# Kernel optimization log

Measured on AMD Instinct MI355X. Metric: run time of the kernel, lower is better.

The kernel has to match this reference:

```python
import jax, jax.numpy as jnp
import numpy as np

B, N, F_IN, F_OUT = 8, 2048, 256, 128
ALPHA = 0.2  # LeakyReLU negative slope (smooth=False)
MASK_VAL = -9e15


def setup_inputs() -> dict:
    key = jax.random.key(0)
    k1, k2, k3, k4 = jax.random.split(key, 4)
    h = jax.random.normal(k1, (B, N, F_IN), dtype=jnp.float32)
    adj = jax.random.randint(k2, (B, N, N), 0, 2, dtype=jnp.int32)
    # xavier_uniform with gain=1.414 ~ U(-b, b), b = gain*sqrt(6/(fan_in+fan_out))
    bW = 1.414 * np.sqrt(6.0 / (F_IN + F_OUT))
    W = jax.random.uniform(k3, (F_IN, F_OUT), minval=-bW, maxval=bW, dtype=jnp.float32)
    ba = 1.414 * np.sqrt(6.0 / (2 * F_OUT + 1))
    a = jax.random.uniform(k4, (2 * F_OUT, 1), minval=-ba, maxval=ba, dtype=jnp.float32)
    return {"h": h, "adj": adj, "W": W, "a": a}


def reference(h, adj, W, a):
    Wh = jnp.einsum('bni,io->bno', h, W)              # [B,N,F_OUT]
    fo = Wh.shape[-1]
    a1 = a[:fo, 0]                                    # attends to source i
    a2 = a[fo:, 0]                                    # attends to target j
    # e[b,i,j] = leaky_relu(Wh[b,i]@a1 + Wh[b,j]@a2) — equivalent to the
    # concat([Wh_i, Wh_j]) @ a construction without the O(N^2 * 2F) tensor.
    s1 = Wh @ a1                                      # [B,N]
    s2 = Wh @ a2                                      # [B,N]
    e = jax.nn.leaky_relu(s1[:, :, None] + s2[:, None, :], negative_slope=ALPHA)
    att = jnp.where(adj > 0, e, MASK_VAL)
    att = jax.nn.softmax(att, axis=-1)                # [B,N,N]
    # dropout is identity in eval mode (training=False)
    h_prime = jnp.einsum('bij,bjo->bio', att, Wh)     # [B,N,F_OUT]
    return jax.nn.elu(h_prime)                        # concat=True path
```

## Files before the change

kernel.cpp:

```cpp
#include <hip/hip_runtime.h>
#include <math.h>

#define Bn 8
#define Nn 2048
#define FIn 256
#define FOn 128

typedef __attribute__((ext_vector_type(8))) short short8;
typedef __attribute__((ext_vector_type(4))) float f32x4;
typedef __attribute__((ext_vector_type(4))) unsigned short ushort4v;

__device__ __forceinline__ unsigned short f2bf(float x){
    union { float f; unsigned u; } v; v.f = x;
    unsigned r = v.u + 0x7fffu + ((v.u >> 16) & 1u);
    return (unsigned short)(r >> 16);
}

__global__ void k0_wt(const float* __restrict__ W, unsigned short* __restrict__ WT){
    int o = blockIdx.x, k = threadIdx.x;
    WT[o*FIn + k] = f2bf(W[k*FOn + o]);
}

__global__ __launch_bounds__(256) void k1_gemm(const float* __restrict__ h,
        const unsigned short* __restrict__ WT, const float* __restrict__ a,
        unsigned short* __restrict__ WhT, float* __restrict__ s1, float* __restrict__ s2){
    __shared__ __align__(16) unsigned short tr[128][48];
    __shared__ float ps1[2][32], ps2[2][32];
    int t = threadIdx.x, lane = t & 63, w = t >> 6;
    int rg = w >> 1, ch = w & 1;
    int l16 = lane & 15, khalf = (lane >> 4) * 8;
    long g0 = (long)blockIdx.x * 32;
    int b = (int)(g0 >> 11);
    int i0 = (int)(g0 & 2047);
    long row = g0 + rg*16 + l16;
    f32x4 acc[4];
    #pragma unroll
    for (int nf=0;nf<4;nf++) acc[nf] = (f32x4){0.f,0.f,0.f,0.f};
    #pragma unroll
    for (int ks=0; ks<8; ks++){
        int kb = ks*32 + khalf;
        const float4* hp = (const float4*)(h + row*FIn + kb);
        float4 h0 = hp[0], h1 = hp[1];
        short8 af;
        af[0]=(short)f2bf(h0.x); af[1]=(short)f2bf(h0.y); af[2]=(short)f2bf(h0.z); af[3]=(short)f2bf(h0.w);
        af[4]=(short)f2bf(h1.x); af[5]=(short)f2bf(h1.y); af[6]=(short)f2bf(h1.z); af[7]=(short)f2bf(h1.w);
        #pragma unroll
        for (int nf=0;nf<4;nf++){
            short8 bfv = *(const short8*)(WT + (ch*64 + nf*16 + l16)*FIn + kb);
            acc[nf] = __builtin_amdgcn_mfma_f32_16x16x32_bf16(af, bfv, acc[nf], 0, 0, 0);
        }
    }
    {
        float a1v[4], a2v[4];
        #pragma unroll
        for (int nf=0;nf<4;nf++){
            a1v[nf] = a[ch*64 + nf*16 + l16];
            a2v[nf] = a[FOn + ch*64 + nf*16 + l16];
        }
        #pragma unroll
        for (int r=0;r<4;r++){
            float u1 = 0.f, u2 = 0.f;
            #pragma unroll
            for (int nf=0;nf<4;nf++){ u1 = fmaf(acc[nf][r], a1v[nf], u1); u2 = fmaf(acc[nf][r], a2v[nf], u2); }
            u1 += __shfl_xor(u1, 1); u1 += __shfl_xor(u1, 2); u1 += __shfl_xor(u1, 4); u1 += __shfl_xor(u1, 8);
            u2 += __shfl_xor(u2, 1); u2 += __shfl_xor(u2, 2); u2 += __shfl_xor(u2, 4); u2 += __shfl_xor(u2, 8);
            if (l16 == 0){
                int rloc = rg*16 + ((lane>>4)<<2) + r;
                ps1[ch][rloc] = u1; ps2[ch][rloc] = u2;
            }
        }
    }
    int rbase = rg*16 + ((lane>>4)<<2);
    #pragma unroll
    for (int nf=0;nf<4;nf++)
        #pragma unroll
        for (int r=0;r<4;r++)
            tr[ch*64 + nf*16 + l16][rbase + r] = f2bf(acc[nf][r]);
    __syncthreads();
    if (t < 32){
        s1[g0 + t] = ps1[0][t] + ps1[1][t];
        s2[g0 + t] = ps2[0][t] + ps2[1][t];
    }
    int o = t >> 1, seg = t & 1;
    short8 v0 = *(const short8*)&tr[o][seg*16];
    short8 v1 = *(const short8*)&tr[o][seg*16 + 8];
    unsigned short* dst = WhT + ((long)(b*FOn + o))*Nn + i0 + seg*16;
    *(short8*)(dst)     = v0;
    *(short8*)(dst + 8) = v1;
}

__global__ __launch_bounds__(512) void k3_flash(const int* __restrict__ adj,
        const unsigned short* __restrict__ WhT, const float* __restrict__ s1g,
        const float* __restrict__ s2g, float* __restrict__ out){
    __shared__ __align__(16) unsigned short pt[2][32][72];
    __shared__ float m_s[32], l_s[32], rs_s[2][32];
    int t = threadIdx.x, lane = t & 63, w = t >> 6;
    int bid = blockIdx.x;
    int b = bid & 7;
    int i0 = (bid >> 3) * 32;
    int q = t >> 4;
    int c = t & 15;
    int rg = w >> 2, cq = w & 3;
    int l16 = lane & 15, khalf = (lane >> 4) * 8;
    if (t < 32){ m_s[t] = -INFINITY; l_s[t] = 0.f; }
    f32x4 acc[2];
    acc[0] = (f32x4){0.f,0.f,0.f,0.f};
    acc[1] = (f32x4){0.f,0.f,0.f,0.f};
    float s1r = s1g[b*Nn + i0 + q];
    const int* ajbase = adj + ((long)(b*Nn + i0 + q))*Nn + c*4;
    const float* s2base = s2g + b*Nn + c*4;
    const unsigned short* Bbase = WhT + ((long)(b*FOn + cq*32 + l16))*Nn + khalf;
    int4 ajA = *(const int4*)(ajbase + 0*64);
    int4 ajB = *(const int4*)(ajbase + 1*64);
    __syncthreads();

#define SCORE_TILE(AJREG, PAR, J0)                                              \
    {                                                                           \
        int4 av = AJREG;                                                        \
        int jn2 = (J0) + 128;  jn2 = jn2 < Nn ? jn2 : Nn - 64;                  \
        AJREG = *(const int4*)(ajbase + jn2);                                   \
        float4 s2c = *(const float4*)(s2base + (J0));                           \
        float sc0 = s1r + s2c.x; sc0 = sc0 > 0.f ? sc0 : 0.2f*sc0; sc0 = av.x > 0 ? sc0 : -9e15f; \
        float sc1 = s1r + s2c.y; sc1 = sc1 > 0.f ? sc1 : 0.2f*sc1; sc1 = av.y > 0 ? sc1 : -9e15f; \
        float sc2 = s1r + s2c.z; sc2 = sc2 > 0.f ? sc2 : 0.2f*sc2; sc2 = av.z > 0 ? sc2 : -9e15f; \
        float sc3 = s1r + s2c.w; sc3 = sc3 > 0.f ? sc3 : 0.2f*sc3; sc3 = av.w > 0 ? sc3 : -9e15f; \
        float tm = fmaxf(fmaxf(sc0, sc1), fmaxf(sc2, sc3));                     \
        tm = fmaxf(tm, __shfl_xor(tm, 1));                                      \
        tm = fmaxf(tm, __shfl_xor(tm, 2));                                      \
        tm = fmaxf(tm, __shfl_xor(tm, 4));                                      \
        tm = fmaxf(tm, __shfl_xor(tm, 8));                                      \
        float mo = m_s[q];                                                      \
        float mn = fmaxf(mo, tm);                                               \
        float rsc = __expf(mo - mn);                                            \
        float p0 = __expf(sc0 - mn), p1 = __expf(sc1 - mn);                     \
        float p2 = __expf(sc2 - mn), p3 = __expf(sc3 - mn);                     \
        float ps = (p0+p1)+(p2+p3);                                             \
        ps += __shfl_xor(ps, 1); ps += __shfl_xor(ps, 2);                       \
        ps += __shfl_xor(ps, 4); ps += __shfl_xor(ps, 8);                       \
        if (c == 0){ m_s[q] = mn; l_s[q] = l_s[q]*rsc + ps; rs_s[PAR][q] = rsc; } \
        ushort4v pv;                                                            \
        pv[0] = f2bf(p0); pv[1] = f2bf(p1); pv[2] = f2bf(p2); pv[3] = f2bf(p3); \
        *(ushort4v*)&pt[PAR][q][c*4] = pv;                                      \
    }

#define MFMA_TILE(PAR, J0)                                                      \
    {                                                                           \
        __syncthreads();                                                        \
        float rv0 = rs_s[PAR][rg*16 + ((lane>>4)<<2) + 0];                      \
        float rv1 = rs_s[PAR][rg*16 + ((lane>>4)<<2) + 1];                      \
        float rv2 = rs_s[PAR][rg*16 + ((lane>>4)<<2) + 2];                      \
        float rv3 = rs_s[PAR][rg*16 + ((lane>>4)<<2) + 3];                      \
        acc[0][0]*=rv0; acc[0][1]*=rv1; acc[0][2]*=rv2; acc[0][3]*=rv3;         \
        acc[1][0]*=rv0; acc[1][1]*=rv1; acc[1][2]*=rv2; acc[1][3]*=rv3;         \
        const unsigned short* Bp = Bbase + (J0);                                \
        _Pragma("unroll")                                                       \
        for (int kk=0;kk<2;kk++){                                               \
            short8 af = *(const short8*)&pt[PAR][rg*16 + l16][kk*32 + khalf];   \
            short8 b0 = *(const short8*)(Bp + kk*32);                           \
            short8 b1 = *(const short8*)(Bp + 16*Nn + kk*32);                   \
            acc[0] = __builtin_amdgcn_mfma_f32_16x16x32_bf16(af, b0, acc[0], 0, 0, 0); \
            acc[1] = __builtin_amdgcn_mfma_f32_16x16x32_bf16(af, b1, acc[1], 0, 0, 0); \
        }                                                                       \
    }

    #pragma unroll 1
    for (int pr = 0; pr < 16; pr++){
        int j0 = pr*128;
        SCORE_TILE(ajA, 0, j0)
        MFMA_TILE(0, j0)
        SCORE_TILE(ajB, 1, j0 + 64)
        MFMA_TILE(1, j0 + 64)
    }
#undef SCORE_TILE
#undef MFMA_TILE

    __syncthreads();
    int rb = rg*16 + ((lane>>4)<<2);
    #pragma unroll
    for (int reg=0;reg<4;reg++){
        int r = rb + reg;
        float inv = 1.f / l_s[r];
        #pragma unroll
        for (int nf=0;nf<2;nf++){
            float v = acc[nf][reg] * inv;
            v = v > 0.f ? v : (__expf(v) - 1.f);
            out[((long)(b*Nn + i0 + r))*FOn + cq*32 + nf*16 + l16] = v;
        }
    }
}

extern "C" void kernel_launch(void* const* d_in, const int* in_sizes, int n_in,
                              void* d_out, int out_size, void* d_ws, size_t ws_size,
                              hipStream_t stream){
    const float* h  = (const float*)d_in[0];
    const int* adj  = (const int*)d_in[1];
    const float* W  = (const float*)d_in[2];
    const float* a  = (const float*)d_in[3];
    float* out = (float*)d_out;
    char* ws = (char*)d_ws;
    unsigned short* WT  = (unsigned short*)(ws);
    unsigned short* WhT = (unsigned short*)(ws + 65536);
    float* s1           = (float*)(ws + 65536 + 4194304);
    float* s2           = (float*)(ws + 65536 + 4194304 + 65536);

    k0_wt   <<<128, 256, 0, stream>>>(W, WT);
    k1_gemm <<<512, 256, 0, stream>>>(h, WT, a, WhT, s1, s2);
    k3_flash<<<512, 512, 0, stream>>>(adj, WhT, s1, s2, out);
}
```

Measured before the change: 262.3 us.

## Stage WhT tiles in shared memory with register-prefetched double buffering

Each block now loads the 128x64 WhT tile cooperatively with coalesced 16-byte loads, prefetching the next tile into registers and storing it into a double-buffered LDS array. MFMA B operands then come from LDS instead of strided global loads duplicated across waves. s2 is also cached in LDS once per block. This costs about 45KB of extra shared memory, which may reduce occupancy.

```diff
diff --git a/kernel.cpp b/kernel.cpp
--- a/kernel.cpp
+++ b/kernel.cpp
@@ -92,7 +92,9 @@
 __global__ __launch_bounds__(512) void k3_flash(const int* __restrict__ adj,
         const unsigned short* __restrict__ WhT, const float* __restrict__ s1g,
         const float* __restrict__ s2g, float* __restrict__ out){
+    __shared__ __align__(16) unsigned short vt[2][128][72];
     __shared__ __align__(16) unsigned short pt[2][32][72];
+    __shared__ float s2t[Nn];
     __shared__ float m_s[32], l_s[32], rs_s[2][32];
     int t = threadIdx.x, lane = t & 63, w = t >> 6;
     int bid = blockIdx.x;
@@ -103,78 +105,72 @@
     int rg = w >> 2, cq = w & 3;
     int l16 = lane & 15, khalf = (lane >> 4) * 8;
     if (t < 32){ m_s[t] = -INFINITY; l_s[t] = 0.f; }
+    *(float4*)&s2t[t*4] = *(const float4*)(s2g + b*Nn + t*4);
     f32x4 acc[2];
     acc[0] = (f32x4){0.f,0.f,0.f,0.f};
     acc[1] = (f32x4){0.f,0.f,0.f,0.f};
     float s1r = s1g[b*Nn + i0 + q];
     const int* ajbase = adj + ((long)(b*Nn + i0 + q))*Nn + c*4;
-    const float* s2base = s2g + b*Nn + c*4;
-    const unsigned short* Bbase = WhT + ((long)(b*FOn + cq*32 + l16))*Nn + khalf;
-    int4 ajA = *(const int4*)(ajbase + 0*64);
-    int4 ajB = *(const int4*)(ajbase + 1*64);
+    int vrow = t >> 3, vj = (t & 7) * 8;
+    const unsigned short* vp0 = WhT + ((long)(b*FOn + vrow))*Nn + vj;
+    const unsigned short* vp1 = vp0 + 64*Nn;
+    short8 vA0 = *(const short8*)(vp0);
+    short8 vA1 = *(const short8*)(vp1);
+    int4 ajA = *(const int4*)(ajbase);
+    int4 ajB = *(const int4*)(ajbase + 64);
     __syncthreads();
 
-#define SCORE_TILE(AJREG, PAR, J0)                                              \
-    {                                                                           \
-        int4 av = AJREG;                                                        \
-        int jn2 = (J0) + 128;  jn2 = jn2 < Nn ? jn2 : Nn - 64;                  \
-        AJREG = *(const int4*)(ajbase + jn2);                                   \
-        float4 s2c = *(const float4*)(s2base + (J0));                           \
-        float sc0 = s1r + s2c.x; sc0 = sc0 > 0.f ? sc0 : 0.2f*sc0; sc0 = av.x > 0 ? sc0 : -9e15f; \
-        float sc1 = s1r + s2c.y; sc1 = sc1 > 0.f ? sc1 : 0.2f*sc1; sc1 = av.y > 0 ? sc1 : -9e15f; \
-        float sc2 = s1r + s2c.z; sc2 = sc2 > 0.f ? sc2 : 0.2f*sc2; sc2 = av.z > 0 ? sc2 : -9e15f; \
-        float sc3 = s1r + s2c.w; sc3 = sc3 > 0.f ? sc3 : 0.2f*sc3; sc3 = av.w > 0 ? sc3 : -9e15f; \
-        float tm = fmaxf(fmaxf(sc0, sc1), fmaxf(sc2, sc3));                     \
-        tm = fmaxf(tm, __shfl_xor(tm, 1));                                      \
-        tm = fmaxf(tm, __shfl_xor(tm, 2));                                      \
-        tm = fmaxf(tm, __shfl_xor(tm, 4));                                      \
-        tm = fmaxf(tm, __shfl_xor(tm, 8));                                      \
-        float mo = m_s[q];                                                      \
-        float mn = fmaxf(mo, tm);                                               \
-        float rsc = __expf(mo - mn);                                            \
-        float p0 = __expf(sc0 - mn), p1 = __expf(sc1 - mn);                     \
-        float p2 = __expf(sc2 - mn), p3 = __expf(sc3 - mn);                     \
-        float ps = (p0+p1)+(p2+p3);                                             \
-        ps += __shfl_xor(ps, 1); ps += __shfl_xor(ps, 2);                       \
-        ps += __shfl_xor(ps, 4); ps += __shfl_xor(ps, 8);                       \
-        if (c == 0){ m_s[q] = mn; l_s[q] = l_s[q]*rsc + ps; rs_s[PAR][q] = rsc; } \
-        ushort4v pv;                                                            \
-        pv[0] = f2bf(p0); pv[1] = f2bf(p1); pv[2] = f2bf(p2); pv[3] = f2bf(p3); \
-        *(ushort4v*)&pt[PAR][q][c*4] = pv;                                      \
-    }
-
-#define MFMA_TILE(PAR, J0)                                                      \
-    {                                                                           \
-        __syncthreads();                                                        \
-        float rv0 = rs_s[PAR][rg*16 + ((lane>>4)<<2) + 0];                      \
-        float rv1 = rs_s[PAR][rg*16 + ((lane>>4)<<2) + 1];                      \
-        float rv2 = rs_s[PAR][rg*16 + ((lane>>4)<<2) + 2];                      \
-        float rv3 = rs_s[PAR][rg*16 + ((lane>>4)<<2) + 3];                      \
-        acc[0][0]*=rv0; acc[0][1]*=rv1; acc[0][2]*=rv2; acc[0][3]*=rv3;         \
-        acc[1][0]*=rv0; acc[1][1]*=rv1; acc[1][2]*=rv2; acc[1][3]*=rv3;         \
-        const unsigned short* Bp = Bbase + (J0);                                \
-        _Pragma("unroll")                                                       \
-        for (int kk=0;kk<2;kk++){                                               \
-            short8 af = *(const short8*)&pt[PAR][rg*16 + l16][kk*32 + khalf];   \
-            short8 b0 = *(const short8*)(Bp + kk*32);                           \
-            short8 b1 = *(const short8*)(Bp + 16*Nn + kk*32);                   \
-            acc[0] = __builtin_amdgcn_mfma_f32_16x16x32_bf16(af, b0, acc[0], 0, 0, 0); \
-            acc[1] = __builtin_amdgcn_mfma_f32_16x16x32_bf16(af, b1, acc[1], 0, 0, 0); \
-        }                                                                       \
-    }
-
     #pragma unroll 1
-    for (int pr = 0; pr < 16; pr++){
-        int j0 = pr*128;
-        SCORE_TILE(ajA, 0, j0)
-        MFMA_TILE(0, j0)
-        SCORE_TILE(ajB, 1, j0 + 64)
-        MFMA_TILE(1, j0 + 64)
-    }
-#undef SCORE_TILE
-#undef MFMA_TILE
-
-    __syncthreads();
+    for (int jt = 0; jt < 32; jt++){
+        int j0 = jt*64;
+        int par = jt & 1;
+        *(short8*)&vt[par][vrow][vj]      = vA0;
+        *(short8*)&vt[par][vrow + 64][vj] = vA1;
+        int jn = (jt < 31) ? j0 + 64 : j0;
+        vA0 = *(const short8*)(vp0 + jn);
+        vA1 = *(const short8*)(vp1 + jn);
+        int4 av = ajA; ajA = ajB;
+        int jn2 = (jt < 30) ? j0 + 128 : j0;
+        ajB = *(const int4*)(ajbase + jn2);
+        float4 s2c = *(const float4*)&s2t[j0 + c*4];
+        float sc0 = s1r + s2c.x; sc0 = sc0 > 0.f ? sc0 : 0.2f*sc0; sc0 = av.x > 0 ? sc0 : -9e15f;
+        float sc1 = s1r + s2c.y; sc1 = sc1 > 0.f ? sc1 : 0.2f*sc1; sc1 = av.y > 0 ? sc1 : -9e15f;
+        float sc2 = s1r + s2c.z; sc2 = sc2 > 0.f ? sc2 : 0.2f*sc2; sc2 = av.z > 0 ? sc2 : -9e15f;
+        float sc3 = s1r + s2c.w; sc3 = sc3 > 0.f ? sc3 : 0.2f*sc3; sc3 = av.w > 0 ? sc3 : -9e15f;
+        float tm = fmaxf(fmaxf(sc0, sc1), fmaxf(sc2, sc3));
+        tm = fmaxf(tm, __shfl_xor(tm, 1));
+        tm = fmaxf(tm, __shfl_xor(tm, 2));
+        tm = fmaxf(tm, __shfl_xor(tm, 4));
+        tm = fmaxf(tm, __shfl_xor(tm, 8));
+        float mo = m_s[q];
+        float mn = fmaxf(mo, tm);
+        float rsc = __expf(mo - mn);
+        float p0 = __expf(sc0 - mn), p1 = __expf(sc1 - mn);
+        float p2 = __expf(sc2 - mn), p3 = __expf(sc3 - mn);
+        float ps = (p0+p1)+(p2+p3);
+        ps += __shfl_xor(ps, 1); ps += __shfl_xor(ps, 2);
+        ps += __shfl_xor(ps, 4); ps += __shfl_xor(ps, 8);
+        if (c == 0){ m_s[q] = mn; l_s[q] = l_s[q]*rsc + ps; rs_s[par][q] = rsc; }
+        ushort4v pv;
+        pv[0] = f2bf(p0); pv[1] = f2bf(p1); pv[2] = f2bf(p2); pv[3] = f2bf(p3);
+        *(ushort4v*)&pt[par][q][c*4] = pv;
+        __syncthreads();
+        int rb = rg*16 + ((lane>>4)<<2);
+        float rv0 = rs_s[par][rb + 0];
+        float rv1 = rs_s[par][rb + 1];
+        float rv2 = rs_s[par][rb + 2];
+        float rv3 = rs_s[par][rb + 3];
+        acc[0][0]*=rv0; acc[0][1]*=rv1; acc[0][2]*=rv2; acc[0][3]*=rv3;
+        acc[1][0]*=rv0; acc[1][1]*=rv1; acc[1][2]*=rv2; acc[1][3]*=rv3;
+        #pragma unroll
+        for (int kk=0;kk<2;kk++){
+            short8 af = *(const short8*)&pt[par][rg*16 + l16][kk*32 + khalf];
+            short8 b0 = *(const short8*)&vt[par][cq*32 + l16][kk*32 + khalf];
+            short8 b1 = *(const short8*)&vt[par][cq*32 + 16 + l16][kk*32 + khalf];
+            acc[0] = __builtin_amdgcn_mfma_f32_16x16x32_bf16(af, b0, acc[0], 0, 0, 0);
+            acc[1] = __builtin_amdgcn_mfma_f32_16x16x32_bf16(af, b1, acc[1], 0, 0, 0);
+        }
+    }
     int rb = rg*16 + ((lane>>4)<<2);
     #pragma unroll
     for (int reg=0;reg<4;reg++){
```

Measured after the change: 229.4 us. -12.6%, faster.

## Replace online softmax with precomputed row-max bound and two-phase score/MFMA blocks

Applied to the files above, without the earlier changes.

Adds a small kernel that computes the per-batch max of s2. Because leaky_relu is monotonic, leaky(s1_i + max s2) is an exact upper bound on each row's scores, so the flash kernel drops the online running max, the rescaling and most cross-thread reductions. The attention loop is rebuilt into two large phases: each thread scores 64 consecutive adjacency entries per half and writes bf16 probabilities to a large shared buffer. Then every wave runs MFMAs over 1024 columns with register-prefetched WhT fragments, computing the transposed product. The costs are a much larger shared-memory footprint that limits occupancy, fewer overlap points between loads and math, and a risk of precision loss when the bound sits far above a row's actual max. Fully masked rows would also get a zero denominator.

```diff
diff --git a/kernel.cpp b/kernel.cpp
--- a/kernel.cpp
+++ b/kernel.cpp
@@ -8,7 +8,6 @@
 
 typedef __attribute__((ext_vector_type(8))) short short8;
 typedef __attribute__((ext_vector_type(4))) float f32x4;
-typedef __attribute__((ext_vector_type(4))) unsigned short ushort4v;
 
 __device__ __forceinline__ unsigned short f2bf(float x){
     union { float f; unsigned u; } v; v.f = x;
@@ -89,104 +88,127 @@
     *(short8*)(dst + 8) = v1;
 }
 
-__global__ __launch_bounds__(512) void k3_flash(const int* __restrict__ adj,
+__global__ __launch_bounds__(256) void k2_s2max(const float* __restrict__ s2, float* __restrict__ s2m){
+    __shared__ float red[4];
+    int b = blockIdx.x, t = threadIdx.x;
+    float m = -1e30f;
+    #pragma unroll
+    for (int k=0;k<8;k++) m = fmaxf(m, s2[b*Nn + t + k*256]);
+    m = fmaxf(m, __shfl_xor(m, 1));
+    m = fmaxf(m, __shfl_xor(m, 2));
+    m = fmaxf(m, __shfl_xor(m, 4));
+    m = fmaxf(m, __shfl_xor(m, 8));
+    m = fmaxf(m, __shfl_xor(m, 16));
+    m = fmaxf(m, __shfl_xor(m, 32));
+    if ((t & 63) == 0) red[t >> 6] = m;
+    __syncthreads();
+    if (t == 0) s2m[b] = fmaxf(fmaxf(red[0], red[1]), fmaxf(red[2], red[3]));
+}
+
+__global__ __launch_bounds__(512, 4) void k3_flash(const int* __restrict__ adj,
         const unsigned short* __restrict__ WhT, const float* __restrict__ s1g,
-        const float* __restrict__ s2g, float* __restrict__ out){
-    __shared__ __align__(16) unsigned short pt[2][32][72];
-    __shared__ float m_s[32], l_s[32], rs_s[2][32];
+        const float* __restrict__ s2g, const float* __restrict__ s2m,
+        float* __restrict__ out){
+    __shared__ unsigned int ptf[16*1156];
+    __shared__ float l_s[32];
     int t = threadIdx.x, lane = t & 63, w = t >> 6;
     int bid = blockIdx.x;
     int b = bid & 7;
     int i0 = (bid >> 3) * 32;
-    int q = t >> 4;
-    int c = t & 15;
-    int rg = w >> 2, cq = w & 3;
-    int l16 = lane & 15, khalf = (lane >> 4) * 8;
-    if (t < 32){ m_s[t] = -INFINITY; l_s[t] = 0.f; }
-    f32x4 acc[2];
-    acc[0] = (f32x4){0.f,0.f,0.f,0.f};
-    acc[1] = (f32x4){0.f,0.f,0.f,0.f};
+    int q = t >> 4, c = t & 15;
+    int l16 = lane & 15, hh = lane >> 4;
     float s1r = s1g[b*Nn + i0 + q];
-    const int* ajbase = adj + ((long)(b*Nn + i0 + q))*Nn + c*4;
-    const float* s2base = s2g + b*Nn + c*4;
-    const unsigned short* Bbase = WhT + ((long)(b*FOn + cq*32 + l16))*Nn + khalf;
-    int4 ajA = *(const int4*)(ajbase + 0*64);
-    int4 ajB = *(const int4*)(ajbase + 1*64);
-    __syncthreads();
-
-#define SCORE_TILE(AJREG, PAR, J0)                                              \
+    float Mx = s1r + s2m[b];
+    Mx = fmaxf(Mx, 0.2f*Mx);
+    float lsum = 0.f;
+    f32x4 acc0 = (f32x4){0.f,0.f,0.f,0.f};
+    f32x4 acc1 = (f32x4){0.f,0.f,0.f,0.f};
+    const int*   ajb = adj + ((long)(b*Nn + i0 + q))*Nn + c*64;
+    const float* s2b = s2g + b*Nn + c*64;
+    const unsigned short* Ab = WhT + ((long)(b*FOn + w*16 + l16))*Nn + hh*8;
+    unsigned int pbase = c*1156 + q*36;
+    int4 aj[16];
+
+#define SCORES(SS)                                                              \
     {                                                                           \
-        int4 av = AJREG;                                                        \
-        int jn2 = (J0) + 128;  jn2 = jn2 < Nn ? jn2 : Nn - 64;                  \
-        AJREG = *(const int4*)(ajbase + jn2);                                   \
-        float4 s2c = *(const float4*)(s2base + (J0));                           \
-        float sc0 = s1r + s2c.x; sc0 = sc0 > 0.f ? sc0 : 0.2f*sc0; sc0 = av.x > 0 ? sc0 : -9e15f; \
-        float sc1 = s1r + s2c.y; sc1 = sc1 > 0.f ? sc1 : 0.2f*sc1; sc1 = av.y > 0 ? sc1 : -9e15f; \
-        float sc2 = s1r + s2c.z; sc2 = sc2 > 0.f ? sc2 : 0.2f*sc2; sc2 = av.z > 0 ? sc2 : -9e15f; \
-        float sc3 = s1r + s2c.w; sc3 = sc3 > 0.f ? sc3 : 0.2f*sc3; sc3 = av.w > 0 ? sc3 : -9e15f; \
-        float tm = fmaxf(fmaxf(sc0, sc1), fmaxf(sc2, sc3));                     \
-        tm = fmaxf(tm, __shfl_xor(tm, 1));                                      \
-        tm = fmaxf(tm, __shfl_xor(tm, 2));                                      \
-        tm = fmaxf(tm, __shfl_xor(tm, 4));                                      \
-        tm = fmaxf(tm, __shfl_xor(tm, 8));                                      \
-        float mo = m_s[q];                                                      \
-        float mn = fmaxf(mo, tm);                                               \
-        float rsc = __expf(mo - mn);                                            \
-        float p0 = __expf(sc0 - mn), p1 = __expf(sc1 - mn);                     \
-        float p2 = __expf(sc2 - mn), p3 = __expf(sc3 - mn);                     \
-        float ps = (p0+p1)+(p2+p3);                                             \
-        ps += __shfl_xor(ps, 1); ps += __shfl_xor(ps, 2);                       \
-        ps += __shfl_xor(ps, 4); ps += __shfl_xor(ps, 8);                       \
-        if (c == 0){ m_s[q] = mn; l_s[q] = l_s[q]*rsc + ps; rs_s[PAR][q] = rsc; } \
-        ushort4v pv;                                                            \
-        pv[0] = f2bf(p0); pv[1] = f2bf(p1); pv[2] = f2bf(p2); pv[3] = f2bf(p3); \
-        *(ushort4v*)&pt[PAR][q][c*4] = pv;                                      \
-    }
-
-#define MFMA_TILE(PAR, J0)                                                      \
+        uint4 pw;                                                               \
+        _Pragma("unroll")                                                       \
+        for (int k=0;k<16;k++){                                                 \
+            int4 av = aj[k];                                                    \
+            float4 s2c = *(const float4*)(s2b + (SS)*1024 + k*4);               \
+            float x0 = s1r + s2c.x; x0 = fmaxf(x0, 0.2f*x0);                    \
+            float x1 = s1r + s2c.y; x1 = fmaxf(x1, 0.2f*x1);                    \
+            float x2 = s1r + s2c.z; x2 = fmaxf(x2, 0.2f*x2);                    \
+            float x3 = s1r + s2c.w; x3 = fmaxf(x3, 0.2f*x3);                    \
+            float p0 = av.x > 0 ? __expf(x0 - Mx) : 0.f;                        \
+            float p1 = av.y > 0 ? __expf(x1 - Mx) : 0.f;                        \
+            float p2 = av.z > 0 ? __expf(x2 - Mx) : 0.f;                        \
+            float p3 = av.w > 0 ? __expf(x3 - Mx) : 0.f;                        \
+            lsum += (p0 + p1) + (p2 + p3);                                      \
+            unsigned lo = (unsigned)f2bf(p0) | ((unsigned)f2bf(p1) << 16);      \
+            unsigned hi = (unsigned)f2bf(p2) | ((unsigned)f2bf(p3) << 16);      \
+            if (k & 1){ pw.z = lo; pw.w = hi;                                   \
+                        *(uint4*)&ptf[pbase + (k>>1)*4] = pw; }                 \
+            else      { pw.x = lo; pw.y = hi; }                                 \
+        }                                                                       \
+    }
+
+#define MFMAPH(SS)                                                              \
     {                                                                           \
-        __syncthreads();                                                        \
-        float rv0 = rs_s[PAR][rg*16 + ((lane>>4)<<2) + 0];                      \
-        float rv1 = rs_s[PAR][rg*16 + ((lane>>4)<<2) + 1];                      \
-        float rv2 = rs_s[PAR][rg*16 + ((lane>>4)<<2) + 2];                      \
-        float rv3 = rs_s[PAR][rg*16 + ((lane>>4)<<2) + 3];                      \
-        acc[0][0]*=rv0; acc[0][1]*=rv1; acc[0][2]*=rv2; acc[0][3]*=rv3;         \
-        acc[1][0]*=rv0; acc[1][1]*=rv1; acc[1][2]*=rv2; acc[1][3]*=rv3;         \
-        const unsigned short* Bp = Bbase + (J0);                                \
+        const unsigned short* Abs = Ab + (SS)*1024;                             \
+        short8 pf0[2], pf1[2];                                                  \
+        pf0[0] = *(const short8*)(Abs);         pf1[0] = *(const short8*)(Abs + 32); \
+        pf0[1] = *(const short8*)(Abs + 64);    pf1[1] = *(const short8*)(Abs + 96); \
         _Pragma("unroll")                                                       \
-        for (int kk=0;kk<2;kk++){                                               \
-            short8 af = *(const short8*)&pt[PAR][rg*16 + l16][kk*32 + khalf];   \
-            short8 b0 = *(const short8*)(Bp + kk*32);                           \
-            short8 b1 = *(const short8*)(Bp + 16*Nn + kk*32);                   \
-            acc[0] = __builtin_amdgcn_mfma_f32_16x16x32_bf16(af, b0, acc[0], 0, 0, 0); \
-            acc[1] = __builtin_amdgcn_mfma_f32_16x16x32_bf16(af, b1, acc[1], 0, 0, 0); \
+        for (int jt=0; jt<16; jt++){                                            \
+            short8 cA0 = pf0[jt&1], cA1 = pf1[jt&1];                            \
+            if (jt < 14){                                                       \
+                pf0[jt&1] = *(const short8*)(Abs + (jt+2)*64);                  \
+                pf1[jt&1] = *(const short8*)(Abs + (jt+2)*64 + 32);             \
+            }                                                                   \
+            unsigned bb = jt*1156;                                              \
+            short8 b00 = *(const short8*)&ptf[bb + l16*36 + hh*4];              \
+            short8 b01 = *(const short8*)&ptf[bb + l16*36 + (4+hh)*4];          \
+            short8 b10 = *(const short8*)&ptf[bb + (16+l16)*36 + hh*4];         \
+            short8 b11 = *(const short8*)&ptf[bb + (16+l16)*36 + (4+hh)*4];     \
+            acc0 = __builtin_amdgcn_mfma_f32_16x16x32_bf16(cA0, b00, acc0, 0, 0, 0); \
+            acc0 = __builtin_amdgcn_mfma_f32_16x16x32_bf16(cA1, b01, acc0, 0, 0, 0); \
+            acc1 = __builtin_amdgcn_mfma_f32_16x16x32_bf16(cA0, b10, acc1, 0, 0, 0); \
+            acc1 = __builtin_amdgcn_mfma_f32_16x16x32_bf16(cA1, b11, acc1, 0, 0, 0); \
         }                                                                       \
     }
 
-    #pragma unroll 1
-    for (int pr = 0; pr < 16; pr++){
-        int j0 = pr*128;
-        SCORE_TILE(ajA, 0, j0)
-        MFMA_TILE(0, j0)
-        SCORE_TILE(ajB, 1, j0 + 64)
-        MFMA_TILE(1, j0 + 64)
-    }
-#undef SCORE_TILE
-#undef MFMA_TILE
-
-    __syncthreads();
-    int rb = rg*16 + ((lane>>4)<<2);
-    #pragma unroll
-    for (int reg=0;reg<4;reg++){
-        int r = rb + reg;
-        float inv = 1.f / l_s[r];
-        #pragma unroll
-        for (int nf=0;nf<2;nf++){
-            float v = acc[nf][reg] * inv;
-            v = v > 0.f ? v : (__expf(v) - 1.f);
-            out[((long)(b*Nn + i0 + r))*FOn + cq*32 + nf*16 + l16] = v;
-        }
-    }
+    #pragma unroll
+    for (int k=0;k<16;k++) aj[k] = *(const int4*)(ajb + k*4);
+    SCORES(0)
+    #pragma unroll
+    for (int k=0;k<16;k++) aj[k] = *(const int4*)(ajb + 1024 + k*4);
+    __syncthreads();
+    MFMAPH(0)
+    __syncthreads();
+    SCORES(1)
+    lsum += __shfl_xor(lsum, 1);
+    lsum += __shfl_xor(lsum, 2);
+    lsum += __shfl_xor(lsum, 4);
+    lsum += __shfl_xor(lsum, 8);
+    if (c == 0) l_s[q] = lsum;
+    __syncthreads();
+    MFMAPH(1)
+#undef SCORES
+#undef MFMAPH
+
+    float li0 = 1.f / l_s[l16];
+    float li1 = 1.f / l_s[16 + l16];
+    float4 o0, o1;
+    #pragma unroll
+    for (int r=0;r<4;r++){
+        float v0 = acc0[r] * li0;
+        float v1 = acc1[r] * li1;
+        ((float*)&o0)[r] = v0 > 0.f ? v0 : (__expf(v0) - 1.f);
+        ((float*)&o1)[r] = v1 > 0.f ? v1 : (__expf(v1) - 1.f);
+    }
+    *(float4*)(out + ((long)(b*Nn + i0 + l16))*FOn + w*16 + hh*4)      = o0;
+    *(float4*)(out + ((long)(b*Nn + i0 + 16 + l16))*FOn + w*16 + hh*4) = o1;
 }
 
 extern "C" void kernel_launch(void* const* d_in, const int* in_sizes, int n_in,
@@ -202,8 +224,10 @@
     unsigned short* WhT = (unsigned short*)(ws + 65536);
     float* s1           = (float*)(ws + 65536 + 4194304);
     float* s2           = (float*)(ws + 65536 + 4194304 + 65536);
-
-    k0_wt   <<<128, 256, 0, stream>>>(W, WT);
-    k1_gemm <<<512, 256, 0, stream>>>(h, WT, a, WhT, s1, s2);
-    k3_flash<<<512, 512, 0, stream>>>(adj, WhT, s1, s2, out);
-}
+    float* s2m          = (float*)(ws + 65536 + 4194304 + 131072);
+
+    k0_wt    <<<128, 256, 0, stream>>>(W, WT);
+    k1_gemm  <<<512, 256, 0, stream>>>(h, WT, a, WhT, s1, s2);
+    k2_s2max <<<Bn,  256, 0, stream>>>(s2, s2m);
+    k3_flash <<<512, 512, 0, stream>>>(adj, WhT, s1, s2, s2m, out);
+}
```

Result: no change. 262.9 us (+0.2%).
